# Kernel optimization log

Hardware: AMD Instinct MI355X
Metric: run time of the kernel (lower is better)

Reference implementation:

```python
import jax, jax.numpy as jnp
import numpy as np

N = 50000
IN, HID, OUT, HEADS = 128, 64, 64, 4


def seg_softmax(logits, seg, num):
    # softmax over edges grouped by destination node; logits [E, H]
    m = jax.ops.segment_max(logits, seg, num_segments=num)
    e = jnp.exp(logits - m[seg])
    s = jax.ops.segment_sum(e, seg, num_segments=num)
    return e / (s[seg] + 1e-16)


def gat_conv(x, src, dst, W, a_s, a_d, b, heads, concat):
    n = x.shape[0]
    h = (x @ W.T).reshape(n, heads, -1)           # [N, H, C]
    alpha_src = jnp.einsum('nhc,hc->nh', h, a_s)   # per-node src score
    alpha_dst = jnp.einsum('nhc,hc->nh', h, a_d)
    logits = jax.nn.leaky_relu(alpha_src[src] + alpha_dst[dst], 0.2)  # [E, H]
    alpha = seg_softmax(logits, dst, n)
    out = jax.ops.segment_sum(alpha[:, :, None] * h[src], dst, num_segments=n)  # [N, H, C]
    out = out.reshape(n, -1) if concat else out.mean(axis=1)
    return out + b


def setup_inputs():
    key = jax.random.key(0)
    ks = jax.random.split(key, 16)
    x = jax.random.normal(ks[0], (N, IN), dtype=jnp.float32)
    edge_index = jax.random.randint(ks[1], (2, 800000), 0, N, dtype=jnp.int64)

    def glorot(k, shape):
        fan = shape[-1]
        return jax.random.normal(k, shape, dtype=jnp.float32) / jnp.sqrt(jnp.float32(fan))

    d = {"x": x, "edge_index": edge_index}
    # layer 1: IN -> HID, HEADS heads, concat
    d["W1"] = glorot(ks[2], (HEADS * HID, IN))
    d["as1"] = glorot(ks[3], (HEADS, HID))
    d["ad1"] = glorot(ks[4], (HEADS, HID))
    d["b1"] = jnp.zeros((HEADS * HID,), jnp.float32)
    # layer 2: HID*HEADS -> HID, HEADS heads, concat
    d["W2"] = glorot(ks[5], (HEADS * HID, HEADS * HID))
    d["as2"] = glorot(ks[6], (HEADS, HID))
    d["ad2"] = glorot(ks[7], (HEADS, HID))
    d["b2"] = jnp.zeros((HEADS * HID,), jnp.float32)
    # layer 3: HID*HEADS -> OUT, 1 head
    d["W3"] = glorot(ks[8], (OUT, HEADS * HID))
    d["as3"] = glorot(ks[9], (1, OUT))
    d["ad3"] = glorot(ks[10], (1, OUT))
    d["b3"] = jnp.zeros((OUT,), jnp.float32)
    return d


def reference(x, edge_index, W1, as1, ad1, b1, W2, as2, ad2, b2, W3, as3, ad3, b3):
    # PyG GATConv adds self-loops by default
    loops = jnp.arange(N, dtype=edge_index.dtype)
    src = jnp.concatenate([edge_index[0], loops])
    dst = jnp.concatenate([edge_index[1], loops])

    h = jax.nn.relu(gat_conv(x, src, dst, W1, as1, ad1, b1, HEADS, True))
    h = jax.nn.relu(gat_conv(h, src, dst, W2, as2, ad2, b2, HEADS, True))
    out = gat_conv(h, src, dst, W3, as3, ad3, b3, 1, True)
    return out
```

## Files before the change

kernel.cpp:

```cpp
#include <hip/hip_runtime.h>
#include <hip/hip_bf16.h>
#include <math.h>


typedef float f32x4 __attribute__((ext_vector_type(4)));
typedef _Float16 half8v __attribute__((ext_vector_type(8)));
typedef _Float16 half4v __attribute__((ext_vector_type(4)));

#define MPAD 50048
#define QINV 2048.0f
#define QDQ  4.8828125e-4f

__device__ __forceinline__ void gload_lds16(const void* g, void* l) {
  __builtin_amdgcn_global_load_lds(
      (const __attribute__((address_space(1))) unsigned int*)g,
      (__attribute__((address_space(3))) unsigned int*)l, 16, 0, 0);
}

__device__ __forceinline__ float leaky02(float l) {
  return (l >= 0.f) ? l : 0.2f * l;
}

__device__ __forceinline__ short quant16(float v) {
  int q = (int)rintf(v * QINV);
  q = q > 32767 ? 32767 : (q < -32768 ? -32768 : q);
  return (short)q;
}


__global__ void hist_kernel(const int* __restrict__ dst, int e, int* counts) {
  int i = blockIdx.x * blockDim.x + threadIdx.x;
  if (i < e) atomicAdd(&counts[dst[i]], 1);
}

__global__ __launch_bounds__(1024) void block_sum_kernel(const int* __restrict__ counts,
                                                         int* __restrict__ bsum, int n) {
  __shared__ int red[1024];
  int i = blockIdx.x * 1024 + threadIdx.x;
  red[threadIdx.x] = (i < n) ? (counts[i] + 1) : 0;
  __syncthreads();
  #pragma unroll
  for (int off = 512; off > 0; off >>= 1) {
    if (threadIdx.x < off) red[threadIdx.x] += red[threadIdx.x + off];
    __syncthreads();
  }
  if (threadIdx.x == 0) bsum[blockIdx.x] = red[0];
}

__global__ void scan_sums_kernel(int* bsum, int nb) {
  int t = threadIdx.x;
  int c = (t < nb) ? bsum[t] : 0;
  int v = c;
  #pragma unroll
  for (int off = 1; off < 64; off <<= 1) {
    int u = __shfl_up(v, off);
    if (t >= off) v += u;
  }
  if (t < nb) bsum[t] = v - c;
}

__global__ __launch_bounds__(1024) void scan_final_kernel(const int* __restrict__ counts,
    const int* __restrict__ bsum, int* __restrict__ offsets, int* __restrict__ cursor, int n) {
  __shared__ int sc[1024];
  int i = blockIdx.x * 1024 + threadIdx.x;
  int c = (i < n) ? (counts[i] + 1) : 0;
  sc[threadIdx.x] = c;
  __syncthreads();
  for (int off = 1; off < 1024; off <<= 1) {
    int v = 0;
    if (threadIdx.x >= off) v = sc[threadIdx.x - off];
    __syncthreads();
    sc[threadIdx.x] += v;
    __syncthreads();
  }
  int excl = sc[threadIdx.x] - c + bsum[blockIdx.x];
  if (i < n) {
    offsets[i] = excl;
    cursor[i] = excl;
  } else if (i == n) {
    offsets[n] = excl;
  }
}

__global__ void scatter_kernel(const int* __restrict__ src, const int* __restrict__ dst,
                               int e800, int etot, int* cursor, int* __restrict__ ssrc) {
  int i = blockIdx.x * blockDim.x + threadIdx.x;
  if (i >= etot) return;
  int s, d;
  if (i < e800) { s = src[i]; d = dst[i]; }
  else          { s = i - e800; d = s; }
  int pos = atomicAdd(&cursor[d], 1);
  ssrc[pos] = s;
}

__global__ void cvt_all_kernel(const float* __restrict__ x, const float* __restrict__ W1,
                               const float* __restrict__ W2, const float* __restrict__ W3,
                               _Float16* __restrict__ x16, _Float16* __restrict__ o1,
                               _Float16* __restrict__ o2, _Float16* __restrict__ o3, int nx4) {
  int i = blockIdx.x * blockDim.x + threadIdx.x;
  const float* in;
  _Float16* out;
  int j;
  if (i < nx4)                       { in = x;  out = x16; j = i; }
  else if ((j = i - nx4) < 8192)     { in = W1; out = o1; }
  else if ((j -= 8192) < 16384)      { in = W2; out = o2; }
  else if ((j -= 16384) < 4096)      { in = W3; out = o3; }
  else return;
  float4 v = reinterpret_cast<const float4*>(in)[j];
  half4v h = {(_Float16)v.x, (_Float16)v.y, (_Float16)v.z, (_Float16)v.w};
  *reinterpret_cast<half4v*>(out + (size_t)j * 4) = h;
}

template <int KP, int BM, int BN, int WAVES_M, int WAVES_N, int OTOT, int HEADS, bool F16OUT>
__global__ __launch_bounds__(256) void gemm2_kernel(
    const _Float16* __restrict__ A, const _Float16* __restrict__ B,
    void* __restrict__ Cq, const float* __restrict__ a_s, const float* __restrict__ a_d,
    float* __restrict__ asrcO, float* __restrict__ adstO, int M) {
  constexpr int BK = 64;
  constexpr int NK = KP / BK;
  constexpr int MFRAG = BM / WAVES_M / 16;
  constexpr int NFRAG = BN / WAVES_N / 16;
  __shared__ _Float16 As[2][BM * BK];
  __shared__ _Float16 Bs[2][BN * BK];

  const int tid = threadIdx.x;
  const int lane = tid & 63;
  const int wid = tid >> 6;
  const int m0 = blockIdx.x * BM;
  const int o0 = blockIdx.y * BN;

  const int srow = tid >> 3;
  const int scolb = (tid & 7) * 16;
  const int sswz = (srow & 7) << 4;
  const char* aSrc = (const char*)A + (size_t)(m0 + srow) * (KP * 2) + (scolb ^ sswz);
  const char* bSrc = (const char*)B + (size_t)(o0 + srow) * (KP * 2) + (scolb ^ sswz);
  char* aDst0 = (char*)&As[0][0] + wid * 1024;
  char* bDst0 = (char*)&Bs[0][0] + wid * 1024;

  auto stage = [&](int buf, int kt) {
    const size_t ko = (size_t)kt * 128;
    char* ad = aDst0 + buf * (BM * 128);
    #pragma unroll
    for (int i = 0; i < BM / 32; ++i)
      gload_lds16(aSrc + ko + (size_t)i * 32 * (KP * 2), ad + i * 4096);
    char* bd = bDst0 + buf * (BN * 128);
    #pragma unroll
    for (int j = 0; j < BN / 32; ++j)
      gload_lds16(bSrc + ko + (size_t)j * 32 * (KP * 2), bd + j * 4096);
  };

  const int fr = lane & 15;
  const int fg = lane >> 4;
  const int fswz = (fr & 7) << 4;
  const int wm0 = (wid / WAVES_N) * (BM / WAVES_M);
  const int wn0 = (wid % WAVES_N) * (BN / WAVES_N);

  f32x4 acc[MFRAG][NFRAG];
  #pragma unroll
  for (int mi = 0; mi < MFRAG; ++mi)
    #pragma unroll
    for (int ni = 0; ni < NFRAG; ++ni) acc[mi][ni] = (f32x4)0.f;

  stage(0, 0);
  __syncthreads();

  for (int kt = 0; kt < NK; ++kt) {
    const int buf = kt & 1;
    if (kt + 1 < NK) stage(buf ^ 1, kt + 1);
    const char* asB = (const char*)&As[buf][0] + (wm0 + fr) * 128;
    const char* bsB = (const char*)&Bs[buf][0] + (wn0 + fr) * 128;
    #pragma unroll
    for (int kh = 0; kh < 2; ++kh) {
      const int kb = (kh * 64 + fg * 16) ^ fswz;
      half8v af[MFRAG], bfr[NFRAG];
      #pragma unroll
      for (int mi = 0; mi < MFRAG; ++mi)
        af[mi] = *reinterpret_cast<const half8v*>(asB + mi * 16 * 128 + kb);
      #pragma unroll
      for (int ni = 0; ni < NFRAG; ++ni)
        bfr[ni] = *reinterpret_cast<const half8v*>(bsB + ni * 16 * 128 + kb);
      #pragma unroll
      for (int mi = 0; mi < MFRAG; ++mi)
        #pragma unroll
        for (int ni = 0; ni < NFRAG; ++ni)
          acc[mi][ni] = __builtin_amdgcn_mfma_f32_16x16x32_f16(af[mi], bfr[ni], acc[mi][ni], 0, 0, 0);
    }
    __syncthreads();
  }

  const int head = (HEADS == 4) ? ((o0 + wn0) >> 6) : 0;
  float asl[NFRAG], adl[NFRAG];
  #pragma unroll
  for (int ni = 0; ni < NFRAG; ++ni) {
    int c64 = (HEADS == 4) ? (ni * 16 + fr) : (wn0 + ni * 16 + fr);
    asl[ni] = a_s[head * 64 + c64];
    adl[ni] = a_d[head * 64 + c64];
  }
  #pragma unroll
  for (int mi = 0; mi < MFRAG; ++mi) {
    #pragma unroll
    for (int r = 0; r < 4; ++r) {
      int row = m0 + wm0 + mi * 16 + fg * 4 + r;
      float ps = 0.f, pd = 0.f;
      #pragma unroll
      for (int ni = 0; ni < NFRAG; ++ni) {
        ps = fmaf(acc[mi][ni][r], asl[ni], ps);
        pd = fmaf(acc[mi][ni][r], adl[ni], pd);
      }
      #pragma unroll
      for (int off = 1; off < 16; off <<= 1) {
        ps += __shfl_xor(ps, off);
        pd += __shfl_xor(pd, off);
      }
      if (row < M) {
        if (fr == 0) {
          asrcO[(size_t)row * HEADS + head] = ps;
          adstO[(size_t)row * HEADS + head] = pd;
        }
        #pragma unroll
        for (int ni = 0; ni < NFRAG; ++ni) {
          size_t ci = (size_t)row * OTOT + o0 + wn0 + ni * 16 + fr;
          if constexpr (F16OUT) ((_Float16*)Cq)[ci] = (_Float16)acc[mi][ni][r];
          else                  ((short*)Cq)[ci] = quant16(acc[mi][ni][r]);
        }
      }
    }
  }
}

__global__ __launch_bounds__(256) void aggregate4_kernel(
    const _Float16* __restrict__ hq, const float* __restrict__ asrc,
    const float* __restrict__ adst, const float* __restrict__ bias,
    const int* __restrict__ offsets, const int* __restrict__ ssrc,
    _Float16* __restrict__ outp, int n) {
  int wid = threadIdx.x >> 6;
  int lane = threadIdx.x & 63;
  int sub = lane >> 5;
  int hl = lane & 31;
  int node = blockIdx.x * 8 + wid * 2 + sub;
  if (node >= n) return;
  int head = hl >> 3;
  int ch8 = hl * 8;
  float adv = adst[(size_t)node * 4 + head];
  int beg = offsets[node], end = offsets[node + 1];

  float s0 = 0.f, s1 = 0.f, s2 = 0.f, s3 = 0.f;
  float A0[8] = {}, A1[8] = {}, A2[8] = {}, A3[8] = {};
  int e = beg;
  for (; e + 3 < end; e += 4) {
    int c0 = ssrc[e + 0], c1 = ssrc[e + 1], c2 = ssrc[e + 2], c3 = ssrc[e + 3];
    float p0 = __expf(leaky02(asrc[(size_t)c0 * 4 + head] + adv));
    float p1 = __expf(leaky02(asrc[(size_t)c1 * 4 + head] + adv));
    float p2 = __expf(leaky02(asrc[(size_t)c2 * 4 + head] + adv));
    float p3 = __expf(leaky02(asrc[(size_t)c3 * 4 + head] + adv));
    half8v h0 = *reinterpret_cast<const half8v*>(&hq[(size_t)c0 * 256 + ch8]);
    half8v h1 = *reinterpret_cast<const half8v*>(&hq[(size_t)c1 * 256 + ch8]);
    half8v h2 = *reinterpret_cast<const half8v*>(&hq[(size_t)c2 * 256 + ch8]);
    half8v h3 = *reinterpret_cast<const half8v*>(&hq[(size_t)c3 * 256 + ch8]);
    s0 += p0; s1 += p1; s2 += p2; s3 += p3;
    #pragma unroll
    for (int j = 0; j < 8; ++j) {
      A0[j] = fmaf((float)h0[j], p0, A0[j]);
      A1[j] = fmaf((float)h1[j], p1, A1[j]);
      A2[j] = fmaf((float)h2[j], p2, A2[j]);
      A3[j] = fmaf((float)h3[j], p3, A3[j]);
    }
  }
  for (; e < end; ++e) {
    int c0 = ssrc[e];
    float p0 = __expf(leaky02(asrc[(size_t)c0 * 4 + head] + adv));
    half8v h0 = *reinterpret_cast<const half8v*>(&hq[(size_t)c0 * 256 + ch8]);
    s0 += p0;
    #pragma unroll
    for (int j = 0; j < 8; ++j) A0[j] = fmaf((float)h0[j], p0, A0[j]);
  }
  float s = (s0 + s1) + (s2 + s3);
  float A[8];
  #pragma unroll
  for (int j = 0; j < 8; ++j) A[j] = (A0[j] + A1[j]) + (A2[j] + A3[j]);

  float inv = 1.f / (s + 1e-16f);
  float4 bv0 = *reinterpret_cast<const float4*>(&bias[ch8]);
  float4 bv1 = *reinterpret_cast<const float4*>(&bias[ch8 + 4]);
  half8v hv;
  hv[0] = (_Float16)fmaxf(A[0] * inv + bv0.x, 0.f);
  hv[1] = (_Float16)fmaxf(A[1] * inv + bv0.y, 0.f);
  hv[2] = (_Float16)fmaxf(A[2] * inv + bv0.z, 0.f);
  hv[3] = (_Float16)fmaxf(A[3] * inv + bv0.w, 0.f);
  hv[4] = (_Float16)fmaxf(A[4] * inv + bv1.x, 0.f);
  hv[5] = (_Float16)fmaxf(A[5] * inv + bv1.y, 0.f);
  hv[6] = (_Float16)fmaxf(A[6] * inv + bv1.z, 0.f);
  hv[7] = (_Float16)fmaxf(A[7] * inv + bv1.w, 0.f);
  *reinterpret_cast<half8v*>(outp + (size_t)node * 256 + ch8) = hv;
}

__global__ __launch_bounds__(256) void aggregate1_kernel(
    const short* __restrict__ hq, const float* __restrict__ asrc,
    const float* __restrict__ adst, const float* __restrict__ bias,
    const int* __restrict__ offsets, const int* __restrict__ ssrc,
    float* __restrict__ out, int n) {
  int wid = threadIdx.x >> 6;
  int lane = threadIdx.x & 63;
  int node = blockIdx.x * 4 + wid;
  if (node >= n) return;
  int g = lane >> 4;
  int w = lane & 15;
  float adv = adst[node];
  int beg = offsets[node], end = offsets[node + 1];

  float s = 0.f;
  float4 A = {0, 0, 0, 0};
  int e0 = beg;
  for (; e0 + 3 < end; e0 += 4) {
    int src = ssrc[e0 + g];
    float p = __expf(leaky02(asrc[src] + adv));
    short4 q = *reinterpret_cast<const short4*>(&hq[(size_t)src * 64 + w * 4]);
    s += p;
    A.x += p * (float)q.x; A.y += p * (float)q.y;
    A.z += p * (float)q.z; A.w += p * (float)q.w;
  }
  if (e0 + g < end) {
    int src = ssrc[e0 + g];
    float p = __expf(leaky02(asrc[src] + adv));
    short4 q = *reinterpret_cast<const short4*>(&hq[(size_t)src * 64 + w * 4]);
    s += p;
    A.x += p * (float)q.x; A.y += p * (float)q.y;
    A.z += p * (float)q.z; A.w += p * (float)q.w;
  }
  #pragma unroll
  for (int off = 16; off < 64; off <<= 1) {
    s += __shfl_xor(s, off);
    A.x += __shfl_xor(A.x, off);
    A.y += __shfl_xor(A.y, off);
    A.z += __shfl_xor(A.z, off);
    A.w += __shfl_xor(A.w, off);
  }
  if (g == 0) {
    float inv = QDQ / (s + 1e-16f);
    float4 bv = *reinterpret_cast<const float4*>(&bias[w * 4]);
    float4 o;
    o.x = A.x * inv + bv.x;
    o.y = A.y * inv + bv.y;
    o.z = A.z * inv + bv.z;
    o.w = A.w * inv + bv.w;
    *reinterpret_cast<float4*>(&out[(size_t)node * 64 + w * 4]) = o;
  }
}


extern "C" void kernel_launch(void* const* d_in, const int* in_sizes, int n_in,
                              void* d_out, int out_size, void* d_ws, size_t ws_size,
                              hipStream_t stream) {
  const float* x   = (const float*)d_in[0];
  const int*   ei  = (const int*)d_in[1];
  const float* W1  = (const float*)d_in[2];
  const float* as1 = (const float*)d_in[3];
  const float* ad1 = (const float*)d_in[4];
  const float* b1  = (const float*)d_in[5];
  const float* W2  = (const float*)d_in[6];
  const float* as2 = (const float*)d_in[7];
  const float* ad2 = (const float*)d_in[8];
  const float* b2  = (const float*)d_in[9];
  const float* W3  = (const float*)d_in[10];
  const float* as3 = (const float*)d_in[11];
  const float* ad3 = (const float*)d_in[12];
  const float* b3  = (const float*)d_in[13];
  float* out = (float*)d_out;

  const int n    = in_sizes[0] / 128;
  const int e800 = in_sizes[1] / 2;
  const int etot = e800 + n;

  char* ws = (char*)d_ws;
  size_t off = 0;
  auto alloc = [&](size_t bytes) -> void* {
    void* p = ws + off;
    off = (off + bytes + 255) & ~(size_t)255;
    return p;
  };
  _Float16* x16    = (_Float16*)alloc((size_t)MPAD * 128 * 2);
  _Float16* feat16 = (_Float16*)alloc((size_t)MPAD * 256 * 2);
  _Float16* hagg16 = (_Float16*)alloc((size_t)MPAD * 256 * 2);
  short*    featL3 = (short*)alloc((size_t)MPAD * 64 * 2);
  _Float16* w1f    = (_Float16*)alloc((size_t)256 * 128 * 2);
  _Float16* w2f    = (_Float16*)alloc((size_t)256 * 256 * 2);
  _Float16* w3f    = (_Float16*)alloc((size_t)64 * 256 * 2);
  float* asrc    = (float*)alloc((size_t)n * 4 * 4);
  float* adst    = (float*)alloc((size_t)n * 4 * 4);
  int*   ssrc    = (int*)alloc((size_t)(etot + 4) * 4);
  int*   offsets = (int*)alloc((size_t)(n + 1) * 4);
  int*   cursor  = (int*)alloc((size_t)n * 4);
  int*   counts  = (int*)alloc((size_t)n * 4);
  int*   bsum    = (int*)alloc((size_t)64 * 4);

  const int* esrc = ei;
  const int* edst = ei + e800;
  const int nbScan = (n + 1024) / 1024;

  hipMemsetAsync(counts, 0, (size_t)n * 4, stream);
  hist_kernel<<<(e800 + 255) / 256, 256, 0, stream>>>(edst, e800, counts);
  block_sum_kernel<<<nbScan, 1024, 0, stream>>>(counts, bsum, n);
  scan_sums_kernel<<<1, 64, 0, stream>>>(bsum, nbScan);
  scan_final_kernel<<<nbScan, 1024, 0, stream>>>(counts, bsum, offsets, cursor, n);
  scatter_kernel<<<(etot + 255) / 256, 256, 0, stream>>>(esrc, edst, e800, etot, cursor, ssrc);

  const int nx4 = n * 128 / 4;
  cvt_all_kernel<<<(nx4 + 28672 + 255) / 256, 256, 0, stream>>>(
      x, W1, W2, W3, x16, w1f, w2f, w3f, nx4);

  const int mBlocks = MPAD / 128;

  gemm2_kernel<128, 128, 128, 2, 2, 256, 4, true><<<dim3(mBlocks, 2), 256, 0, stream>>>(
      x16, w1f, feat16, as1, ad1, asrc, adst, n);
  aggregate4_kernel<<<(n + 7) / 8, 256, 0, stream>>>(
      feat16, asrc, adst, b1, offsets, ssrc, hagg16, n);

  gemm2_kernel<256, 128, 128, 2, 2, 256, 4, true><<<dim3(mBlocks, 2), 256, 0, stream>>>(
      hagg16, w2f, feat16, as2, ad2, asrc, adst, n);
  aggregate4_kernel<<<(n + 7) / 8, 256, 0, stream>>>(
      feat16, asrc, adst, b2, offsets, ssrc, hagg16, n);

  gemm2_kernel<256, 128, 64, 4, 1, 64, 1, false><<<dim3(mBlocks, 1), 256, 0, stream>>>(
      hagg16, w3f, featL3, as3, ad3, asrc, adst, n);
  aggregate1_kernel<<<(n + 3) / 4, 256, 0, stream>>>(
      featL3, asrc, adst, b3, offsets, ssrc, out, n);
}
```

Before: 330.8 us.

## Fuse CSR build (memset, histogram, scan, scatter) into one cooperative kernel

Replaces the memset plus five separate kernels that build the destination-sorted edge list with a single cooperative kernel of 256 blocks that uses grid-wide syncs between phases. This removes several launch gaps and the memset. The tradeoff is that only 256x256 threads handle the 850k-edge histogram and scatter loops, and each grid.sync adds its own cost. The scan relies on 256*256 covering n=50000, which holds here.

Result: slower. 452.8 us (+36.9%).

```diff
diff --git a/kernel.cpp b/kernel.cpp
--- a/kernel.cpp
+++ b/kernel.cpp
@@ -1,7 +1,10 @@
 #include <hip/hip_runtime.h>
 #include <hip/hip_bf16.h>
+#include <hip/hip_cooperative_groups.h>
 #include <math.h>
 
+
+namespace cg = cooperative_groups;
 
 typedef float f32x4 __attribute__((ext_vector_type(4)));
 typedef _Float16 half8v __attribute__((ext_vector_type(8)));
@@ -27,70 +30,67 @@
   return (short)q;
 }
 
-
-__global__ void hist_kernel(const int* __restrict__ dst, int e, int* counts) {
-  int i = blockIdx.x * blockDim.x + threadIdx.x;
-  if (i < e) atomicAdd(&counts[dst[i]], 1);
-}
-
-__global__ __launch_bounds__(1024) void block_sum_kernel(const int* __restrict__ counts,
-                                                         int* __restrict__ bsum, int n) {
-  __shared__ int red[1024];
-  int i = blockIdx.x * 1024 + threadIdx.x;
-  red[threadIdx.x] = (i < n) ? (counts[i] + 1) : 0;
+__global__ __launch_bounds__(256) void sort_coop_kernel(
+    const int* __restrict__ src, const int* __restrict__ dst,
+    int e800, int etot, int n, int* __restrict__ counts, int* __restrict__ bsum,
+    int* __restrict__ offsets, int* __restrict__ cursor, int* __restrict__ ssrc) {
+  cg::grid_group grid = cg::this_grid();
+  const int t = threadIdx.x;
+  const int gid = blockIdx.x * 256 + t;
+  const int nth = gridDim.x * 256;
+
+  for (int i = gid; i < n; i += nth) counts[i] = 0;
+  grid.sync();
+
+  for (int i = gid; i < e800; i += nth) atomicAdd(&counts[dst[i]], 1);
+  grid.sync();
+
+  __shared__ int sc[256];
+  int c = (gid < n) ? (counts[gid] + 1) : 0;
+  sc[t] = c;
   __syncthreads();
-  #pragma unroll
-  for (int off = 512; off > 0; off >>= 1) {
-    if (threadIdx.x < off) red[threadIdx.x] += red[threadIdx.x + off];
+  for (int off = 1; off < 256; off <<= 1) {
+    int v = 0;
+    if (t >= off) v = sc[t - off];
     __syncthreads();
-  }
-  if (threadIdx.x == 0) bsum[blockIdx.x] = red[0];
-}
-
-__global__ void scan_sums_kernel(int* bsum, int nb) {
-  int t = threadIdx.x;
-  int c = (t < nb) ? bsum[t] : 0;
-  int v = c;
-  #pragma unroll
-  for (int off = 1; off < 64; off <<= 1) {
-    int u = __shfl_up(v, off);
-    if (t >= off) v += u;
-  }
-  if (t < nb) bsum[t] = v - c;
-}
-
-__global__ __launch_bounds__(1024) void scan_final_kernel(const int* __restrict__ counts,
-    const int* __restrict__ bsum, int* __restrict__ offsets, int* __restrict__ cursor, int n) {
-  __shared__ int sc[1024];
-  int i = blockIdx.x * 1024 + threadIdx.x;
-  int c = (i < n) ? (counts[i] + 1) : 0;
-  sc[threadIdx.x] = c;
-  __syncthreads();
-  for (int off = 1; off < 1024; off <<= 1) {
-    int v = 0;
-    if (threadIdx.x >= off) v = sc[threadIdx.x - off];
+    sc[t] += v;
     __syncthreads();
-    sc[threadIdx.x] += v;
+  }
+  int lexcl = sc[t] - c;
+  if (t == 255) bsum[blockIdx.x] = sc[255];
+  grid.sync();
+
+  if (blockIdx.x == 0) {
+    __shared__ int sb[256];
+    int b = bsum[t];
+    sb[t] = b;
     __syncthreads();
-  }
-  int excl = sc[threadIdx.x] - c + bsum[blockIdx.x];
-  if (i < n) {
-    offsets[i] = excl;
-    cursor[i] = excl;
-  } else if (i == n) {
-    offsets[n] = excl;
-  }
-}
-
-__global__ void scatter_kernel(const int* __restrict__ src, const int* __restrict__ dst,
-                               int e800, int etot, int* cursor, int* __restrict__ ssrc) {
-  int i = blockIdx.x * blockDim.x + threadIdx.x;
-  if (i >= etot) return;
-  int s, d;
-  if (i < e800) { s = src[i]; d = dst[i]; }
-  else          { s = i - e800; d = s; }
-  int pos = atomicAdd(&cursor[d], 1);
-  ssrc[pos] = s;
+    for (int off = 1; off < 256; off <<= 1) {
+      int v = 0;
+      if (t >= off) v = sb[t - off];
+      __syncthreads();
+      sb[t] += v;
+      __syncthreads();
+    }
+    bsum[t] = sb[t] - b;
+    if (t == 0) offsets[n] = etot;
+  }
+  grid.sync();
+
+  if (gid < n) {
+    int excl = lexcl + bsum[blockIdx.x];
+    offsets[gid] = excl;
+    cursor[gid] = excl;
+  }
+  grid.sync();
+
+  for (int i = gid; i < etot; i += nth) {
+    int s, d;
+    if (i < e800) { s = src[i]; d = dst[i]; }
+    else          { s = i - e800; d = s; }
+    int pos = atomicAdd(&cursor[d], 1);
+    ssrc[pos] = s;
+  }
 }
 
 __global__ void cvt_all_kernel(const float* __restrict__ x, const float* __restrict__ W1,
@@ -391,18 +391,16 @@
   int*   offsets = (int*)alloc((size_t)(n + 1) * 4);
   int*   cursor  = (int*)alloc((size_t)n * 4);
   int*   counts  = (int*)alloc((size_t)n * 4);
-  int*   bsum    = (int*)alloc((size_t)64 * 4);
+  int*   bsum    = (int*)alloc((size_t)256 * 4);
 
   const int* esrc = ei;
   const int* edst = ei + e800;
-  const int nbScan = (n + 1024) / 1024;
-
-  hipMemsetAsync(counts, 0, (size_t)n * 4, stream);
-  hist_kernel<<<(e800 + 255) / 256, 256, 0, stream>>>(edst, e800, counts);
-  block_sum_kernel<<<nbScan, 1024, 0, stream>>>(counts, bsum, n);
-  scan_sums_kernel<<<1, 64, 0, stream>>>(bsum, nbScan);
-  scan_final_kernel<<<nbScan, 1024, 0, stream>>>(counts, bsum, offsets, cursor, n);
-  scatter_kernel<<<(etot + 255) / 256, 256, 0, stream>>>(esrc, edst, e800, etot, cursor, ssrc);
+
+  {
+    void* args[] = {(void*)&esrc, (void*)&edst, (void*)&e800, (void*)&etot, (void*)&n,
+                    (void*)&counts, (void*)&bsum, (void*)&offsets, (void*)&cursor, (void*)&ssrc};
+    hipLaunchCooperativeKernel((void*)sort_coop_kernel, dim3(256), dim3(256), args, 0, stream);
+  }
 
   const int nx4 = n * 128 / 4;
   cvt_all_kernel<<<(nx4 + 28672 + 255) / 256, 256, 0, stream>>>(
```
